# Performance work log

Hardware: AMD Instinct MI355X
Metric: run time of the kernel (lower is better)

The kernel has to match this reference:

```python
import jax, jax.numpy as jnp
import numpy as np

P = 8          # patch_size
HEADS = 4      # patch_size // 2
DIM = 256      # nf*P*P // 16
DH = DIM // HEADS


def setup_inputs() -> dict:
    key = jax.random.key(0)
    ks = jax.random.split(key, 8)
    B, N, C, H, W = 8, 1, 64, 256, 256
    Np = (H // P) * (W // P)           # 1024
    patch_dim = C * P * P              # 4096
    s = 0.02
    return {
        "x": jax.random.normal(ks[0], (B, N, C, H, W), jnp.float32),
        "W_embed": jax.random.normal(ks[1], (DIM, patch_dim), jnp.float32) * s,
        "b_embed": jnp.zeros((DIM,), jnp.float32),
        "pos": jax.random.normal(ks[2], (1, Np, DIM), jnp.float32),
        "Wq": jax.random.normal(ks[3], (DIM, DIM), jnp.float32) * s,
        "Wk": jax.random.normal(ks[4], (Np, Np), jnp.float32) * s,
        "Wv": jax.random.normal(ks[5], (DIM, DIM), jnp.float32) * s,
        "Wout": jax.random.normal(ks[6], (patch_dim, DIM), jnp.float32) * s,
        "b_out": jnp.zeros((patch_dim,), jnp.float32),
    }


def reference(x, W_embed, b_embed, pos, Wq, Wk, Wv, Wout, b_out):
    B, N, C, H, W = x.shape
    Hp, Wp = H // P, W // P
    Np = Hp * Wp
    patch_dim = C * P * P
    BN = B * N

    # unfold (non-overlapping patches), column order = (C, kh, kw)
    xb = x.reshape(BN, C, Hp, P, Wp, P)
    patches = xb.transpose(0, 2, 4, 1, 3, 5).reshape(BN, Np, patch_dim)

    # linear_embed + positional embedding
    emb = jnp.einsum('bnp,dp->bnd', patches, W_embed) + b_embed + pos  # (BN, Np, DIM)

    # q: linear, split heads, mean over head-dim (AvgPool1d(dh) on length dh)
    q = jnp.einsum('bnd,ed->bne', emb, Wq)
    q = q.reshape(BN, Np, HEADS, DH).transpose(0, 2, 1, 3)  # (BN, H, Np, DH)
    q = q.mean(axis=-1)                                      # (BN, H, Np)

    # k = sigmoid(linear_k(q)); diag_embed(k) @ v == k[..., None] * v
    k = jax.nn.sigmoid(jnp.einsum('bhn,mn->bhm', q, Wk))     # (BN, H, Np)

    v = jnp.einsum('bnd,ed->bne', emb, Wv)
    v = v.reshape(BN, Np, HEADS, DH).transpose(0, 2, 1, 3)   # (BN, H, Np, DH)

    out = k[..., None] * v                                   # (BN, H, Np, DH)
    out = out.transpose(0, 2, 1, 3).reshape(BN, Np, DIM)

    out = jnp.einsum('bnd,pd->bnp', out, Wout) + b_out       # (BN, Np, patch_dim)

    # fold back to image
    out = out.reshape(BN, Hp, Wp, C, P, P).transpose(0, 3, 1, 4, 2, 5)
    out = out.reshape(B, N, C, H, W)
    return out
```

## Files before the change

kernel.cpp:

```cpp
#include <hip/hip_runtime.h>

typedef __attribute__((ext_vector_type(8))) short short8;
typedef __attribute__((ext_vector_type(4))) float f32x4;

#define LDA 72
#define QST 264
#define KST 257

__device__ __forceinline__ unsigned short f2bf(float f) {
  unsigned int u = __builtin_bit_cast(unsigned int, f);
  u += 0x7fffu + ((u >> 16) & 1u);
  return (unsigned short)(u >> 16);
}
__device__ __forceinline__ float bf2f(unsigned short us) {
  return __builtin_bit_cast(float, (unsigned int)us << 16);
}

__global__ __launch_bounds__(256) void cvt_bf16_kernel(const float* __restrict__ src,
                                                       unsigned short* __restrict__ dst,
                                                       int n4) {
  int i = blockIdx.x * 256 + threadIdx.x;
  if (i >= n4) return;
  float4 f = ((const float4*)src)[i];
  unsigned int lo = (unsigned int)f2bf(f.x) | ((unsigned int)f2bf(f.y) << 16);
  unsigned int hi = (unsigned int)f2bf(f.z) | ((unsigned int)f2bf(f.w) << 16);
  uint2 u; u.x = lo; u.y = hi;
  ((uint2*)dst)[i] = u;
}

__global__ __launch_bounds__(256) void wqr_kernel(const float* __restrict__ Wq,
                                                  float* __restrict__ WqR) {
  int idx = blockIdx.x * 256 + threadIdx.x;
  int h = idx >> 8, e = idx & 255;
  float s = 0.f;
  for (int j = 0; j < 64; ++j) s += Wq[(size_t)(h * 64 + j) * 256 + e];
  WqR[idx] = s * (1.f / 64.f);
}

__global__ __launch_bounds__(256) void gemm1_embed(
    const float* __restrict__ x, const unsigned short* __restrict__ Wb,
    const float* __restrict__ b_embed, const float* __restrict__ pos,
    unsigned short* __restrict__ emb_bf) {
  __shared__ __align__(16) unsigned short As[64 * LDA];
  __shared__ __align__(16) unsigned short Bs[128 * LDA];
  const int nt = blockIdx.x, mt = blockIdx.y;
  const int m0 = mt * 64, n0 = nt * 128;
  const int t = threadIdx.x;
  const int wave = t >> 6, lane = t & 63;
  const int wm = wave >> 1, wn = wave & 1;
  const int lr = lane & 15, lq = lane >> 4;
  f32x4 acc[2][4];
#pragma unroll
  for (int i = 0; i < 2; i++)
#pragma unroll
    for (int j = 0; j < 4; j++) acc[i][j] = f32x4{0.f, 0.f, 0.f, 0.f};

  for (int kt = 0; kt < 64; ++kt) {
    const int k0 = kt * 64;
#pragma unroll
    for (int rr = 0; rr < 2; ++rr) {
      int r = t + rr * 256;
      int m = r >> 3, krun = r & 7;
      int gm = m0 + m;
      int bn = gm >> 10, nn = gm & 1023;
      int ph = nn >> 5, pw = nn & 31;
      int k = k0 + krun * 8;
      int c = k >> 6, kh = (k >> 3) & 7;
      const float* src = x + ((size_t)((bn << 6) + c) << 16) +
                         (size_t)((ph << 3) + kh) * 256 + (pw << 3);
      float4 f0 = *(const float4*)src;
      float4 f1 = *(const float4*)(src + 4);
      short8 v;
      v[0] = (short)f2bf(f0.x); v[1] = (short)f2bf(f0.y);
      v[2] = (short)f2bf(f0.z); v[3] = (short)f2bf(f0.w);
      v[4] = (short)f2bf(f1.x); v[5] = (short)f2bf(f1.y);
      v[6] = (short)f2bf(f1.z); v[7] = (short)f2bf(f1.w);
      *(short8*)&As[m * LDA + krun * 8] = v;
    }
#pragma unroll
    for (int rr = 0; rr < 4; ++rr) {
      int r = t + rr * 256;
      int n = r >> 3, krun = r & 7;
      *(short8*)&Bs[n * LDA + krun * 8] =
          *(const short8*)(Wb + (size_t)(n0 + n) * 4096 + k0 + krun * 8);
    }
    __syncthreads();
#pragma unroll
    for (int kc = 0; kc < 2; ++kc) {
      short8 a0 = *(const short8*)&As[(wm * 32 + lr) * LDA + kc * 32 + lq * 8];
      short8 a1 = *(const short8*)&As[(wm * 32 + 16 + lr) * LDA + kc * 32 + lq * 8];
#pragma unroll
      for (int ni = 0; ni < 4; ++ni) {
        short8 b = *(const short8*)&Bs[(wn * 64 + ni * 16 + lr) * LDA + kc * 32 + lq * 8];
        acc[0][ni] = __builtin_amdgcn_mfma_f32_16x16x32_bf16(a0, b, acc[0][ni], 0, 0, 0);
        acc[1][ni] = __builtin_amdgcn_mfma_f32_16x16x32_bf16(a1, b, acc[1][ni], 0, 0, 0);
      }
    }
    __syncthreads();
  }
#pragma unroll
  for (int mi = 0; mi < 2; ++mi)
#pragma unroll
    for (int ni = 0; ni < 4; ++ni) {
      int col = n0 + wn * 64 + ni * 16 + lr;
      float be = b_embed[col];
      int rbase = m0 + wm * 32 + mi * 16 + lq * 4;
#pragma unroll
      for (int r2 = 0; r2 < 4; ++r2) {
        int row = rbase + r2;
        int n = row & 1023;
        emb_bf[(size_t)row * 256 + col] =
            f2bf(acc[mi][ni][r2] + be + pos[(size_t)n * 256 + col]);
      }
    }
}

__global__ __launch_bounds__(256) void q_kernel(const unsigned short* __restrict__ emb_bf,
                                                const float* __restrict__ WqR,
                                                float* __restrict__ q) {
  __shared__ __align__(16) unsigned short es[64 * QST];
  __shared__ float wq[1024];
  const int t = threadIdx.x;
  for (int i = t; i < 1024; i += 256) wq[i] = WqR[i];
  const int row0 = blockIdx.x * 64;
#pragma unroll
  for (int i = 0; i < 8; ++i) {
    int r = t + i * 256;
    int rr = r >> 5, c8 = r & 31;
    *(short8*)&es[rr * QST + c8 * 8] =
        *(const short8*)(emb_bf + (size_t)(row0 + rr) * 256 + c8 * 8);
  }
  __syncthreads();
  const int row = t >> 2, h = t & 3;
  const float* w = wq + h * 256;
  float s = 0.f;
#pragma unroll 4
  for (int e8 = 0; e8 < 32; ++e8) {
    short8 v = *(const short8*)&es[row * QST + e8 * 8];
#pragma unroll
    for (int j = 0; j < 8; ++j)
      s += bf2f((unsigned short)v[j]) * w[e8 * 8 + j];
  }
  int grow = row0 + row;
  int bn = grow >> 10, n = grow & 1023;
  q[(size_t)(bn * 4 + h) * 1024 + n] = s;
}

__global__ __launch_bounds__(256) void k_kernel(const float* __restrict__ q,
                                                const float* __restrict__ Wk,
                                                float* __restrict__ kk) {
  __shared__ float wks[32 * KST];
  __shared__ float qs[32 * KST];
  const int m0 = blockIdx.x * 32;
  const int t = threadIdx.x;
  const int m = t & 31, bh4 = t >> 5;
  float acc[4] = {0.f, 0.f, 0.f, 0.f};
  for (int kt = 0; kt < 4; ++kt) {
    const int k0 = kt * 256;
#pragma unroll
    for (int i = 0; i < 32; ++i) {
      int r = t + i * 256;
      int rr = r >> 8, c = r & 255;
      wks[rr * KST + c] = Wk[(size_t)(m0 + rr) * 1024 + k0 + c];
      qs[rr * KST + c] = q[(size_t)rr * 1024 + k0 + c];
    }
    __syncthreads();
    for (int k = 0; k < 256; ++k) {
      float a = wks[m * KST + k];
      acc[0] += a * qs[(bh4 * 4 + 0) * KST + k];
      acc[1] += a * qs[(bh4 * 4 + 1) * KST + k];
      acc[2] += a * qs[(bh4 * 4 + 2) * KST + k];
      acc[3] += a * qs[(bh4 * 4 + 3) * KST + k];
    }
    __syncthreads();
  }
#pragma unroll
  for (int j = 0; j < 4; ++j)
    kk[(size_t)(bh4 * 4 + j) * 1024 + m0 + m] = 1.f / (1.f + __expf(-acc[j]));
}

__global__ __launch_bounds__(256) void vgemm_kernel(
    const unsigned short* __restrict__ Abf, const unsigned short* __restrict__ Wvb,
    const float* __restrict__ kk, unsigned short* __restrict__ ov) {
  __shared__ __align__(16) unsigned short As[64 * LDA];
  __shared__ __align__(16) unsigned short Bs[64 * LDA];
  const int nt = blockIdx.x, mt = blockIdx.y;
  const int m0 = mt * 64, n0 = nt * 64;
  const int t = threadIdx.x;
  const int wave = t >> 6, lane = t & 63;
  const int wm = wave >> 1, wn = wave & 1;
  const int lr = lane & 15, lq = lane >> 4;
  f32x4 acc[2][2];
#pragma unroll
  for (int i = 0; i < 2; i++)
#pragma unroll
    for (int j = 0; j < 2; j++) acc[i][j] = f32x4{0.f, 0.f, 0.f, 0.f};

  for (int kt = 0; kt < 4; ++kt) {
    const int k0 = kt * 64;
#pragma unroll
    for (int rr = 0; rr < 2; ++rr) {
      int r = t + rr * 256;
      int m = r >> 3, krun = r & 7;
      *(short8*)&As[m * LDA + krun * 8] =
          *(const short8*)(Abf + (size_t)(m0 + m) * 256 + k0 + krun * 8);
    }
#pragma unroll
    for (int rr = 0; rr < 2; ++rr) {
      int r = t + rr * 256;
      int n = r >> 3, krun = r & 7;
      *(short8*)&Bs[n * LDA + krun * 8] =
          *(const short8*)(Wvb + (size_t)(n0 + n) * 256 + k0 + krun * 8);
    }
    __syncthreads();
#pragma unroll
    for (int kc = 0; kc < 2; ++kc) {
      short8 a0 = *(const short8*)&As[(wm * 32 + lr) * LDA + kc * 32 + lq * 8];
      short8 a1 = *(const short8*)&As[(wm * 32 + 16 + lr) * LDA + kc * 32 + lq * 8];
      short8 b0 = *(const short8*)&Bs[(wn * 32 + lr) * LDA + kc * 32 + lq * 8];
      short8 b1 = *(const short8*)&Bs[(wn * 32 + 16 + lr) * LDA + kc * 32 + lq * 8];
      acc[0][0] = __builtin_amdgcn_mfma_f32_16x16x32_bf16(a0, b0, acc[0][0], 0, 0, 0);
      acc[0][1] = __builtin_amdgcn_mfma_f32_16x16x32_bf16(a0, b1, acc[0][1], 0, 0, 0);
      acc[1][0] = __builtin_amdgcn_mfma_f32_16x16x32_bf16(a1, b0, acc[1][0], 0, 0, 0);
      acc[1][1] = __builtin_amdgcn_mfma_f32_16x16x32_bf16(a1, b1, acc[1][1], 0, 0, 0);
    }
    __syncthreads();
  }
#pragma unroll
  for (int mi = 0; mi < 2; ++mi)
#pragma unroll
    for (int ni = 0; ni < 2; ++ni) {
      int col = n0 + wn * 32 + ni * 16 + lr;
      int h = col >> 6;
      int rbase = m0 + wm * 32 + mi * 16 + lq * 4;
#pragma unroll
      for (int r2 = 0; r2 < 4; ++r2) {
        int row = rbase + r2;
        int bn = row >> 10, n = row & 1023;
        float g = kk[(size_t)(bn * 4 + h) * 1024 + n];
        ov[(size_t)row * 256 + col] = f2bf(acc[mi][ni][r2] * g);
      }
    }
}

__global__ __launch_bounds__(256) void gemm2_out(
    const unsigned short* __restrict__ Abf, const unsigned short* __restrict__ Wob,
    const float* __restrict__ b_out, float* __restrict__ out) {
  __shared__ __align__(16) unsigned short As[64 * LDA];
  __shared__ __align__(16) unsigned short Bs[64 * LDA];
  const int nt = blockIdx.x, mt = blockIdx.y;
  const int m0 = mt * 64, n0 = nt * 64;
  const int t = threadIdx.x;
  const int wave = t >> 6, lane = t & 63;
  const int wm = wave >> 1, wn = wave & 1;
  const int lr = lane & 15, lq = lane >> 4;
  f32x4 acc[2][2];
#pragma unroll
  for (int i = 0; i < 2; i++)
#pragma unroll
    for (int j = 0; j < 2; j++) acc[i][j] = f32x4{0.f, 0.f, 0.f, 0.f};

  for (int kt = 0; kt < 4; ++kt) {
    const int k0 = kt * 64;
#pragma unroll
    for (int rr = 0; rr < 2; ++rr) {
      int r = t + rr * 256;
      int m = r >> 3, krun = r & 7;
      *(short8*)&As[m * LDA + krun * 8] =
          *(const short8*)(Abf + (size_t)(m0 + m) * 256 + k0 + krun * 8);
    }
#pragma unroll
    for (int rr = 0; rr < 2; ++rr) {
      int r = t + rr * 256;
      int n = r >> 3, krun = r & 7;
      *(short8*)&Bs[n * LDA + krun * 8] =
          *(const short8*)(Wob + (size_t)(n0 + n) * 256 + k0 + krun * 8);
    }
    __syncthreads();
#pragma unroll
    for (int kc = 0; kc < 2; ++kc) {
      short8 a0 = *(const short8*)&As[(wm * 32 + lr) * LDA + kc * 32 + lq * 8];
      short8 a1 = *(const short8*)&As[(wm * 32 + 16 + lr) * LDA + kc * 32 + lq * 8];
      short8 b0 = *(const short8*)&Bs[(wn * 32 + lr) * LDA + kc * 32 + lq * 8];
      short8 b1 = *(const short8*)&Bs[(wn * 32 + 16 + lr) * LDA + kc * 32 + lq * 8];
      acc[0][0] = __builtin_amdgcn_mfma_f32_16x16x32_bf16(a0, b0, acc[0][0], 0, 0, 0);
      acc[0][1] = __builtin_amdgcn_mfma_f32_16x16x32_bf16(a0, b1, acc[0][1], 0, 0, 0);
      acc[1][0] = __builtin_amdgcn_mfma_f32_16x16x32_bf16(a1, b0, acc[1][0], 0, 0, 0);
      acc[1][1] = __builtin_amdgcn_mfma_f32_16x16x32_bf16(a1, b1, acc[1][1], 0, 0, 0);
    }
    __syncthreads();
  }
#pragma unroll
  for (int mi = 0; mi < 2; ++mi)
#pragma unroll
    for (int ni = 0; ni < 2; ++ni) {
      int p = n0 + wn * 32 + ni * 16 + lr;
      int c = p >> 6, kh = (p >> 3) & 7, kw = p & 7;
      float bo = b_out[p];
      int rbase = m0 + wm * 32 + mi * 16 + lq * 4;
#pragma unroll
      for (int r2 = 0; r2 < 4; ++r2) {
        int row = rbase + r2;
        int bn = row >> 10, nn = row & 1023;
        int ph = nn >> 5, pw = nn & 31;
        size_t addr = ((size_t)((bn << 6) + c) << 16) +
                      (size_t)((ph << 3) + kh) * 256 + (pw << 3) + kw;
        out[addr] = acc[mi][ni][r2] + bo;
      }
    }
}

extern "C" void kernel_launch(void* const* d_in, const int* in_sizes, int n_in,
                              void* d_out, int out_size, void* d_ws, size_t ws_size,
                              hipStream_t stream) {
  const float* x       = (const float*)d_in[0];
  const float* W_embed = (const float*)d_in[1];
  const float* b_embed = (const float*)d_in[2];
  const float* pos     = (const float*)d_in[3];
  const float* Wq      = (const float*)d_in[4];
  const float* Wk      = (const float*)d_in[5];
  const float* Wv      = (const float*)d_in[6];
  const float* Wout    = (const float*)d_in[7];
  const float* b_out   = (const float*)d_in[8];
  float* out = (float*)d_out;

  char* ws = (char*)d_ws;
  const size_t MB = 1024 * 1024;
  unsigned short* emb_bf = (unsigned short*)(ws);
  unsigned short* ov     = (unsigned short*)(ws + 4 * MB);
  unsigned short* Wb     = (unsigned short*)(ws + 8 * MB);
  unsigned short* Wob    = (unsigned short*)(ws + 10 * MB);
  unsigned short* Wvb    = (unsigned short*)(ws + 12 * MB);
  float* q               = (float*)(ws + 12 * MB + 131072);
  float* kk              = (float*)(ws + 12 * MB + 262144);
  float* WqR             = (float*)(ws + 12 * MB + 393216);

  cvt_bf16_kernel<<<1024, 256, 0, stream>>>(W_embed, Wb, 262144);
  cvt_bf16_kernel<<<1024, 256, 0, stream>>>(Wout, Wob, 262144);
  cvt_bf16_kernel<<<64, 256, 0, stream>>>(Wv, Wvb, 16384);
  wqr_kernel<<<4, 256, 0, stream>>>(Wq, WqR);
  gemm1_embed<<<dim3(2, 128), 256, 0, stream>>>(x, Wb, b_embed, pos, emb_bf);
  q_kernel<<<128, 256, 0, stream>>>(emb_bf, WqR, q);
  k_kernel<<<32, 256, 0, stream>>>(q, Wk, kk);
  vgemm_kernel<<<dim3(4, 128), 256, 0, stream>>>(emb_bf, Wvb, kk, ov);
  gemm2_out<<<dim3(64, 128), 256, 0, stream>>>(ov, Wob, b_out, out);
}
```

Baseline: 389.3 us.

## Split-K embed GEMM, fuse reduction with q, retile k/v/out kernels, coalesce output stores

Merges the four weight-prep launches into a single kernel. Splits the embedding GEMM four ways along K so the grid grows from 256 to 1024 blocks, then sums the partials in a new kernel that also adds bias and pos and computes q. The k kernel gets more blocks and float4 loads, vgemm uses 32-row tiles for more blocks, and gemm2 uses 128-wide tiles that are staged through shared memory so the fold back to the image is written with coalesced float4 stores. The cost is extra global traffic for the fp32 partials, about 32MB written and read.

```diff
diff --git a/kernel.cpp b/kernel.cpp
--- a/kernel.cpp
+++ b/kernel.cpp
@@ -4,8 +4,7 @@
 typedef __attribute__((ext_vector_type(4))) float f32x4;
 
 #define LDA 72
-#define QST 264
-#define KST 257
+#define KST 260
 
 __device__ __forceinline__ unsigned short f2bf(float f) {
   unsigned int u = __builtin_bit_cast(unsigned int, f);
@@ -16,11 +15,9 @@
   return __builtin_bit_cast(float, (unsigned int)us << 16);
 }
 
-__global__ __launch_bounds__(256) void cvt_bf16_kernel(const float* __restrict__ src,
-                                                       unsigned short* __restrict__ dst,
-                                                       int n4) {
-  int i = blockIdx.x * 256 + threadIdx.x;
-  if (i >= n4) return;
+__device__ __forceinline__ void cvt_block(const float* __restrict__ src,
+                                          unsigned short* __restrict__ dst, int b) {
+  int i = b * 256 + threadIdx.x;
   float4 f = ((const float4*)src)[i];
   unsigned int lo = (unsigned int)f2bf(f.x) | ((unsigned int)f2bf(f.y) << 16);
   unsigned int hi = (unsigned int)f2bf(f.z) | ((unsigned int)f2bf(f.w) << 16);
@@ -28,9 +25,16 @@
   ((uint2*)dst)[i] = u;
 }
 
-__global__ __launch_bounds__(256) void wqr_kernel(const float* __restrict__ Wq,
-                                                  float* __restrict__ WqR) {
-  int idx = blockIdx.x * 256 + threadIdx.x;
+__global__ __launch_bounds__(256) void prep_kernel(
+    const float* __restrict__ W_embed, const float* __restrict__ Wout,
+    const float* __restrict__ Wv, const float* __restrict__ Wq,
+    unsigned short* __restrict__ Wb, unsigned short* __restrict__ Wob,
+    unsigned short* __restrict__ Wvb, float* __restrict__ WqR) {
+  int b = blockIdx.x;
+  if (b < 1024) { cvt_block(W_embed, Wb, b); return; }
+  if (b < 2048) { cvt_block(Wout, Wob, b - 1024); return; }
+  if (b < 2112) { cvt_block(Wv, Wvb, b - 2048); return; }
+  int idx = (b - 2112) * 256 + threadIdx.x;
   int h = idx >> 8, e = idx & 255;
   float s = 0.f;
   for (int j = 0; j < 64; ++j) s += Wq[(size_t)(h * 64 + j) * 256 + e];
@@ -39,11 +43,10 @@
 
 __global__ __launch_bounds__(256) void gemm1_embed(
     const float* __restrict__ x, const unsigned short* __restrict__ Wb,
-    const float* __restrict__ b_embed, const float* __restrict__ pos,
-    unsigned short* __restrict__ emb_bf) {
+    float* __restrict__ part) {
   __shared__ __align__(16) unsigned short As[64 * LDA];
   __shared__ __align__(16) unsigned short Bs[128 * LDA];
-  const int nt = blockIdx.x, mt = blockIdx.y;
+  const int nt = blockIdx.x, mt = blockIdx.y, sk = blockIdx.z;
   const int m0 = mt * 64, n0 = nt * 128;
   const int t = threadIdx.x;
   const int wave = t >> 6, lane = t & 63;
@@ -55,7 +58,7 @@
 #pragma unroll
     for (int j = 0; j < 4; j++) acc[i][j] = f32x4{0.f, 0.f, 0.f, 0.f};
 
-  for (int kt = 0; kt < 64; ++kt) {
+  for (int kt = sk * 16; kt < sk * 16 + 16; ++kt) {
     const int k0 = kt * 64;
 #pragma unroll
     for (int rr = 0; rr < 2; ++rr) {
@@ -98,103 +101,192 @@
     }
     __syncthreads();
   }
+  float* pdst = part + (size_t)sk * 2097152;
 #pragma unroll
   for (int mi = 0; mi < 2; ++mi)
 #pragma unroll
     for (int ni = 0; ni < 4; ++ni) {
       int col = n0 + wn * 64 + ni * 16 + lr;
-      float be = b_embed[col];
       int rbase = m0 + wm * 32 + mi * 16 + lq * 4;
 #pragma unroll
-      for (int r2 = 0; r2 < 4; ++r2) {
-        int row = rbase + r2;
-        int n = row & 1023;
-        emb_bf[(size_t)row * 256 + col] =
-            f2bf(acc[mi][ni][r2] + be + pos[(size_t)n * 256 + col]);
-      }
-    }
-}
-
-__global__ __launch_bounds__(256) void q_kernel(const unsigned short* __restrict__ emb_bf,
-                                                const float* __restrict__ WqR,
-                                                float* __restrict__ q) {
-  __shared__ __align__(16) unsigned short es[64 * QST];
+      for (int r2 = 0; r2 < 4; ++r2)
+        pdst[(size_t)(rbase + r2) * 256 + col] = acc[mi][ni][r2];
+    }
+}
+
+__global__ __launch_bounds__(256) void finq_kernel(
+    const float* __restrict__ part, const float* __restrict__ b_embed,
+    const float* __restrict__ pos, const float* __restrict__ WqR,
+    unsigned short* __restrict__ emb_bf, float* __restrict__ q) {
   __shared__ float wq[1024];
   const int t = threadIdx.x;
   for (int i = t; i < 1024; i += 256) wq[i] = WqR[i];
-  const int row0 = blockIdx.x * 64;
-#pragma unroll
-  for (int i = 0; i < 8; ++i) {
-    int r = t + i * 256;
-    int rr = r >> 5, c8 = r & 31;
-    *(short8*)&es[rr * QST + c8 * 8] =
-        *(const short8*)(emb_bf + (size_t)(row0 + rr) * 256 + c8 * 8);
-  }
   __syncthreads();
-  const int row = t >> 2, h = t & 3;
-  const float* w = wq + h * 256;
-  float s = 0.f;
-#pragma unroll 4
-  for (int e8 = 0; e8 < 32; ++e8) {
-    short8 v = *(const short8*)&es[row * QST + e8 * 8];
-#pragma unroll
-    for (int j = 0; j < 8; ++j)
-      s += bf2f((unsigned short)v[j]) * w[e8 * 8 + j];
-  }
-  int grow = row0 + row;
-  int bn = grow >> 10, n = grow & 1023;
-  q[(size_t)(bn * 4 + h) * 1024 + n] = s;
+  const int row_l = t >> 3, seg = t & 7;
+  const int row = blockIdx.x * 32 + row_l;
+  const int bn = row >> 10, n = row & 1023;
+  const float4* p4 = (const float4*)part;
+  const float4* b4 = (const float4*)b_embed;
+  const float4* pos4 = (const float4*)pos;
+  const float4* wq4 = (const float4*)wq;
+  const int idx0 = row * 64 + seg * 8;
+
+  float4 e[8];
+#pragma unroll
+  for (int j = 0; j < 8; ++j) {
+    float4 v = p4[idx0 + j];
+    float4 v1 = p4[524288 + idx0 + j];
+    float4 v2 = p4[1048576 + idx0 + j];
+    float4 v3 = p4[1572864 + idx0 + j];
+    float4 bb = b4[seg * 8 + j];
+    float4 pp = pos4[(size_t)n * 64 + seg * 8 + j];
+    e[j].x = v.x + v1.x + v2.x + v3.x + bb.x + pp.x;
+    e[j].y = v.y + v1.y + v2.y + v3.y + bb.y + pp.y;
+    e[j].z = v.z + v1.z + v2.z + v3.z + bb.z + pp.z;
+    e[j].w = v.w + v1.w + v2.w + v3.w + bb.w + pp.w;
+  }
+  unsigned int ub[16];
+#pragma unroll
+  for (int j = 0; j < 8; ++j) {
+    ub[2 * j]     = (unsigned int)f2bf(e[j].x) | ((unsigned int)f2bf(e[j].y) << 16);
+    ub[2 * j + 1] = (unsigned int)f2bf(e[j].z) | ((unsigned int)f2bf(e[j].w) << 16);
+  }
+  uint4* dst = (uint4*)(emb_bf + (size_t)row * 256 + seg * 32);
+#pragma unroll
+  for (int j = 0; j < 4; ++j)
+    dst[j] = make_uint4(ub[4 * j], ub[4 * j + 1], ub[4 * j + 2], ub[4 * j + 3]);
+  float s[4] = {0.f, 0.f, 0.f, 0.f};
+#pragma unroll
+  for (int h = 0; h < 4; ++h)
+#pragma unroll
+    for (int j = 0; j < 8; ++j) {
+      float4 w = wq4[h * 64 + seg * 8 + j];
+      s[h] += e[j].x * w.x + e[j].y * w.y + e[j].z * w.z + e[j].w * w.w;
+    }
+#pragma unroll
+  for (int h = 0; h < 4; ++h) {
+    s[h] += __shfl_xor(s[h], 1);
+    s[h] += __shfl_xor(s[h], 2);
+    s[h] += __shfl_xor(s[h], 4);
+  }
+  if (seg == 0) {
+#pragma unroll
+    for (int h = 0; h < 4; ++h)
+      q[(size_t)(bn * 4 + h) * 1024 + n] = s[h];
+  }
 }
 
 __global__ __launch_bounds__(256) void k_kernel(const float* __restrict__ q,
                                                 const float* __restrict__ Wk,
                                                 float* __restrict__ kk) {
-  __shared__ float wks[32 * KST];
-  __shared__ float qs[32 * KST];
-  const int m0 = blockIdx.x * 32;
-  const int t = threadIdx.x;
-  const int m = t & 31, bh4 = t >> 5;
-  float acc[4] = {0.f, 0.f, 0.f, 0.f};
+  __shared__ float wk_s[8 * KST];
+  __shared__ float q_s[32 * KST];
+  const int m0 = blockIdx.x * 8;
+  const int t = threadIdx.x;
+  const int m = t & 7, bh = t >> 3;
+  const float4* wkg = (const float4*)Wk;
+  const float4* qg = (const float4*)q;
+  float acc = 0.f;
   for (int kt = 0; kt < 4; ++kt) {
     const int k0 = kt * 256;
 #pragma unroll
-    for (int i = 0; i < 32; ++i) {
-      int r = t + i * 256;
-      int rr = r >> 8, c = r & 255;
-      wks[rr * KST + c] = Wk[(size_t)(m0 + rr) * 1024 + k0 + c];
-      qs[rr * KST + c] = q[(size_t)rr * 1024 + k0 + c];
-    }
-    __syncthreads();
-    for (int k = 0; k < 256; ++k) {
-      float a = wks[m * KST + k];
-      acc[0] += a * qs[(bh4 * 4 + 0) * KST + k];
-      acc[1] += a * qs[(bh4 * 4 + 1) * KST + k];
-      acc[2] += a * qs[(bh4 * 4 + 2) * KST + k];
-      acc[3] += a * qs[(bh4 * 4 + 3) * KST + k];
-    }
-    __syncthreads();
-  }
-#pragma unroll
-  for (int j = 0; j < 4; ++j)
-    kk[(size_t)(bh4 * 4 + j) * 1024 + m0 + m] = 1.f / (1.f + __expf(-acc[j]));
+    for (int i = 0; i < 2; ++i) {
+      int idx = t + i * 256;
+      int r = idx >> 6, c4 = idx & 63;
+      *(float4*)&wk_s[r * KST + c4 * 4] = wkg[((size_t)(m0 + r) * 1024 + k0) / 4 + c4];
+    }
+#pragma unroll
+    for (int i = 0; i < 8; ++i) {
+      int idx = t + i * 256;
+      int r = idx >> 6, c4 = idx & 63;
+      *(float4*)&q_s[r * KST + c4 * 4] = qg[((size_t)r * 1024 + k0) / 4 + c4];
+    }
+    __syncthreads();
+#pragma unroll 8
+    for (int k4 = 0; k4 < 64; ++k4) {
+      float4 a = *(const float4*)&wk_s[m * KST + k4 * 4];
+      float4 b = *(const float4*)&q_s[bh * KST + k4 * 4];
+      acc += a.x * b.x + a.y * b.y + a.z * b.z + a.w * b.w;
+    }
+    __syncthreads();
+  }
+  kk[(size_t)bh * 1024 + m0 + m] = 1.f / (1.f + __expf(-acc));
 }
 
 __global__ __launch_bounds__(256) void vgemm_kernel(
     const unsigned short* __restrict__ Abf, const unsigned short* __restrict__ Wvb,
     const float* __restrict__ kk, unsigned short* __restrict__ ov) {
-  __shared__ __align__(16) unsigned short As[64 * LDA];
+  __shared__ __align__(16) unsigned short As[32 * LDA];
   __shared__ __align__(16) unsigned short Bs[64 * LDA];
   const int nt = blockIdx.x, mt = blockIdx.y;
-  const int m0 = mt * 64, n0 = nt * 64;
+  const int m0 = mt * 32, n0 = nt * 64;
+  const int t = threadIdx.x;
+  const int wave = t >> 6, lane = t & 63;
+  const int wr = wave >> 1, wc = wave & 1;
+  const int lr = lane & 15, lq = lane >> 4;
+  f32x4 acc[2];
+  acc[0] = f32x4{0.f, 0.f, 0.f, 0.f};
+  acc[1] = f32x4{0.f, 0.f, 0.f, 0.f};
+
+  for (int kt = 0; kt < 4; ++kt) {
+    const int k0 = kt * 64;
+    {
+      int m = t >> 3, krun = t & 7;
+      *(short8*)&As[m * LDA + krun * 8] =
+          *(const short8*)(Abf + (size_t)(m0 + m) * 256 + k0 + krun * 8);
+    }
+#pragma unroll
+    for (int rr = 0; rr < 2; ++rr) {
+      int r = t + rr * 256;
+      int n = r >> 3, krun = r & 7;
+      *(short8*)&Bs[n * LDA + krun * 8] =
+          *(const short8*)(Wvb + (size_t)(n0 + n) * 256 + k0 + krun * 8);
+    }
+    __syncthreads();
+#pragma unroll
+    for (int kc = 0; kc < 2; ++kc) {
+      short8 a = *(const short8*)&As[(wr * 16 + lr) * LDA + kc * 32 + lq * 8];
+#pragma unroll
+      for (int ni = 0; ni < 2; ++ni) {
+        short8 b = *(const short8*)&Bs[(wc * 32 + ni * 16 + lr) * LDA + kc * 32 + lq * 8];
+        acc[ni] = __builtin_amdgcn_mfma_f32_16x16x32_bf16(a, b, acc[ni], 0, 0, 0);
+      }
+    }
+    __syncthreads();
+  }
+#pragma unroll
+  for (int ni = 0; ni < 2; ++ni) {
+    int col = n0 + wc * 32 + ni * 16 + lr;
+    int h = col >> 6;
+    int rbase = m0 + wr * 16 + lq * 4;
+#pragma unroll
+    for (int r2 = 0; r2 < 4; ++r2) {
+      int row = rbase + r2;
+      int bn = row >> 10, n = row & 1023;
+      float g = kk[(size_t)(bn * 4 + h) * 1024 + n];
+      ov[(size_t)row * 256 + col] = f2bf(acc[ni][r2] * g);
+    }
+  }
+}
+
+#define CST 132
+__global__ __launch_bounds__(256) void gemm2_out(
+    const unsigned short* __restrict__ Abf, const unsigned short* __restrict__ Wob,
+    const float* __restrict__ b_out, float* __restrict__ out) {
+  __shared__ __align__(16) float smem[64 * CST];
+  unsigned short* As = (unsigned short*)smem;
+  unsigned short* Bs = As + 64 * LDA;
+  const int nt = blockIdx.x, mt = blockIdx.y;
+  const int m0 = mt * 64, n0 = nt * 128;
   const int t = threadIdx.x;
   const int wave = t >> 6, lane = t & 63;
   const int wm = wave >> 1, wn = wave & 1;
   const int lr = lane & 15, lq = lane >> 4;
-  f32x4 acc[2][2];
+  f32x4 acc[2][4];
 #pragma unroll
   for (int i = 0; i < 2; i++)
 #pragma unroll
-    for (int j = 0; j < 2; j++) acc[i][j] = f32x4{0.f, 0.f, 0.f, 0.f};
+    for (int j = 0; j < 4; j++) acc[i][j] = f32x4{0.f, 0.f, 0.f, 0.f};
 
   for (int kt = 0; kt < 4; ++kt) {
     const int k0 = kt * 64;
@@ -206,108 +298,57 @@
           *(const short8*)(Abf + (size_t)(m0 + m) * 256 + k0 + krun * 8);
     }
 #pragma unroll
-    for (int rr = 0; rr < 2; ++rr) {
+    for (int rr = 0; rr < 4; ++rr) {
       int r = t + rr * 256;
       int n = r >> 3, krun = r & 7;
       *(short8*)&Bs[n * LDA + krun * 8] =
-          *(const short8*)(Wvb + (size_t)(n0 + n) * 256 + k0 + krun * 8);
+          *(const short8*)(Wob + (size_t)(n0 + n) * 256 + k0 + krun * 8);
     }
     __syncthreads();
 #pragma unroll
     for (int kc = 0; kc < 2; ++kc) {
       short8 a0 = *(const short8*)&As[(wm * 32 + lr) * LDA + kc * 32 + lq * 8];
       short8 a1 = *(const short8*)&As[(wm * 32 + 16 + lr) * LDA + kc * 32 + lq * 8];
-      short8 b0 = *(const short8*)&Bs[(wn * 32 + lr) * LDA + kc * 32 + lq * 8];
-      short8 b1 = *(const short8*)&Bs[(wn * 32 + 16 + lr) * LDA + kc * 32 + lq * 8];
-      acc[0][0] = __builtin_amdgcn_mfma_f32_16x16x32_bf16(a0, b0, acc[0][0], 0, 0, 0);
-      acc[0][1] = __builtin_amdgcn_mfma_f32_16x16x32_bf16(a0, b1, acc[0][1], 0, 0, 0);
-      acc[1][0] = __builtin_amdgcn_mfma_f32_16x16x32_bf16(a1, b0, acc[1][0], 0, 0, 0);
-      acc[1][1] = __builtin_amdgcn_mfma_f32_16x16x32_bf16(a1, b1, acc[1][1], 0, 0, 0);
+#pragma unroll
+      for (int ni = 0; ni < 4; ++ni) {
+        short8 b = *(const short8*)&Bs[(wn * 64 + ni * 16 + lr) * LDA + kc * 32 + lq * 8];
+        acc[0][ni] = __builtin_amdgcn_mfma_f32_16x16x32_bf16(a0, b, acc[0][ni], 0, 0, 0);
+        acc[1][ni] = __builtin_amdgcn_mfma_f32_16x16x32_bf16(a1, b, acc[1][ni], 0, 0, 0);
+      }
     }
     __syncthreads();
   }
 #pragma unroll
   for (int mi = 0; mi < 2; ++mi)
 #pragma unroll
-    for (int ni = 0; ni < 2; ++ni) {
-      int col = n0 + wn * 32 + ni * 16 + lr;
-      int h = col >> 6;
-      int rbase = m0 + wm * 32 + mi * 16 + lq * 4;
-#pragma unroll
-      for (int r2 = 0; r2 < 4; ++r2) {
-        int row = rbase + r2;
-        int bn = row >> 10, n = row & 1023;
-        float g = kk[(size_t)(bn * 4 + h) * 1024 + n];
-        ov[(size_t)row * 256 + col] = f2bf(acc[mi][ni][r2] * g);
-      }
-    }
-}
-
-__global__ __launch_bounds__(256) void gemm2_out(
-    const unsigned short* __restrict__ Abf, const unsigned short* __restrict__ Wob,
-    const float* __restrict__ b_out, float* __restrict__ out) {
-  __shared__ __align__(16) unsigned short As[64 * LDA];
-  __shared__ __align__(16) unsigned short Bs[64 * LDA];
-  const int nt = blockIdx.x, mt = blockIdx.y;
-  const int m0 = mt * 64, n0 = nt * 64;
-  const int t = threadIdx.x;
-  const int wave = t >> 6, lane = t & 63;
-  const int wm = wave >> 1, wn = wave & 1;
-  const int lr = lane & 15, lq = lane >> 4;
-  f32x4 acc[2][2];
-#pragma unroll
-  for (int i = 0; i < 2; i++)
-#pragma unroll
-    for (int j = 0; j < 2; j++) acc[i][j] = f32x4{0.f, 0.f, 0.f, 0.f};
-
-  for (int kt = 0; kt < 4; ++kt) {
-    const int k0 = kt * 64;
-#pragma unroll
-    for (int rr = 0; rr < 2; ++rr) {
-      int r = t + rr * 256;
-      int m = r >> 3, krun = r & 7;
-      *(short8*)&As[m * LDA + krun * 8] =
-          *(const short8*)(Abf + (size_t)(m0 + m) * 256 + k0 + krun * 8);
-    }
-#pragma unroll
-    for (int rr = 0; rr < 2; ++rr) {
-      int r = t + rr * 256;
-      int n = r >> 3, krun = r & 7;
-      *(short8*)&Bs[n * LDA + krun * 8] =
-          *(const short8*)(Wob + (size_t)(n0 + n) * 256 + k0 + krun * 8);
-    }
-    __syncthreads();
-#pragma unroll
-    for (int kc = 0; kc < 2; ++kc) {
-      short8 a0 = *(const short8*)&As[(wm * 32 + lr) * LDA + kc * 32 + lq * 8];
-      short8 a1 = *(const short8*)&As[(wm * 32 + 16 + lr) * LDA + kc * 32 + lq * 8];
-      short8 b0 = *(const short8*)&Bs[(wn * 32 + lr) * LDA + kc * 32 + lq * 8];
-      short8 b1 = *(const short8*)&Bs[(wn * 32 + 16 + lr) * LDA + kc * 32 + lq * 8];
-      acc[0][0] = __builtin_amdgcn_mfma_f32_16x16x32_bf16(a0, b0, acc[0][0], 0, 0, 0);
-      acc[0][1] = __builtin_amdgcn_mfma_f32_16x16x32_bf16(a0, b1, acc[0][1], 0, 0, 0);
-      acc[1][0] = __builtin_amdgcn_mfma_f32_16x16x32_bf16(a1, b0, acc[1][0], 0, 0, 0);
-      acc[1][1] = __builtin_amdgcn_mfma_f32_16x16x32_bf16(a1, b1, acc[1][1], 0, 0, 0);
-    }
-    __syncthreads();
-  }
-#pragma unroll
-  for (int mi = 0; mi < 2; ++mi)
-#pragma unroll
-    for (int ni = 0; ni < 2; ++ni) {
-      int p = n0 + wn * 32 + ni * 16 + lr;
-      int c = p >> 6, kh = (p >> 3) & 7, kw = p & 7;
-      float bo = b_out[p];
-      int rbase = m0 + wm * 32 + mi * 16 + lq * 4;
-#pragma unroll
-      for (int r2 = 0; r2 < 4; ++r2) {
-        int row = rbase + r2;
-        int bn = row >> 10, nn = row & 1023;
-        int ph = nn >> 5, pw = nn & 31;
-        size_t addr = ((size_t)((bn << 6) + c) << 16) +
-                      (size_t)((ph << 3) + kh) * 256 + (pw << 3) + kw;
-        out[addr] = acc[mi][ni][r2] + bo;
-      }
-    }
+    for (int ni = 0; ni < 4; ++ni) {
+      int pl = wn * 64 + ni * 16 + lr;
+      int mb = wm * 32 + mi * 16 + lq * 4;
+#pragma unroll
+      for (int r2 = 0; r2 < 4; ++r2)
+        smem[(mb + r2) * CST + pl] = acc[mi][ni][r2];
+    }
+  __syncthreads();
+  const int bn = m0 >> 10;
+  const int ph0 = (m0 & 1023) >> 5;
+  const int c0 = n0 >> 6;
+#pragma unroll
+  for (int i = 0; i < 8; ++i) {
+    int idx4 = t + i * 256;
+    int kw4 = idx4 & 1;
+    int pw = (idx4 >> 1) & 31;
+    int kh = (idx4 >> 6) & 7;
+    int c2 = (idx4 >> 9) & 1;
+    int ph = (idx4 >> 10) & 1;
+    int m_local = ph * 32 + pw;
+    int p_local = c2 * 64 + kh * 8 + kw4 * 4;
+    float4 v = *(const float4*)&smem[m_local * CST + p_local];
+    float4 bo = *(const float4*)(b_out + n0 + p_local);
+    v.x += bo.x; v.y += bo.y; v.z += bo.z; v.w += bo.w;
+    size_t addr = ((size_t)((bn << 6) + c0 + c2) << 16) +
+                  (size_t)(((ph0 + ph) << 3) + kh) * 256 + (pw << 3) + kw4 * 4;
+    *(float4*)(out + addr) = v;
+  }
 }
 
 extern "C" void kernel_launch(void* const* d_in, const int* in_sizes, int n_in,
@@ -326,22 +367,20 @@
 
   char* ws = (char*)d_ws;
   const size_t MB = 1024 * 1024;
-  unsigned short* emb_bf = (unsigned short*)(ws);
-  unsigned short* ov     = (unsigned short*)(ws + 4 * MB);
-  unsigned short* Wb     = (unsigned short*)(ws + 8 * MB);
-  unsigned short* Wob    = (unsigned short*)(ws + 10 * MB);
-  unsigned short* Wvb    = (unsigned short*)(ws + 12 * MB);
-  float* q               = (float*)(ws + 12 * MB + 131072);
-  float* kk              = (float*)(ws + 12 * MB + 262144);
-  float* WqR             = (float*)(ws + 12 * MB + 393216);
-
-  cvt_bf16_kernel<<<1024, 256, 0, stream>>>(W_embed, Wb, 262144);
-  cvt_bf16_kernel<<<1024, 256, 0, stream>>>(Wout, Wob, 262144);
-  cvt_bf16_kernel<<<64, 256, 0, stream>>>(Wv, Wvb, 16384);
-  wqr_kernel<<<4, 256, 0, stream>>>(Wq, WqR);
-  gemm1_embed<<<dim3(2, 128), 256, 0, stream>>>(x, Wb, b_embed, pos, emb_bf);
-  q_kernel<<<128, 256, 0, stream>>>(emb_bf, WqR, q);
-  k_kernel<<<32, 256, 0, stream>>>(q, Wk, kk);
-  vgemm_kernel<<<dim3(4, 128), 256, 0, stream>>>(emb_bf, Wvb, kk, ov);
-  gemm2_out<<<dim3(64, 128), 256, 0, stream>>>(ov, Wob, b_out, out);
-}
+  float* part            = (float*)(ws);
+  unsigned short* ov     = (unsigned short*)(ws);
+  unsigned short* emb_bf = (unsigned short*)(ws + 32 * MB);
+  unsigned short* Wb     = (unsigned short*)(ws + 36 * MB);
+  unsigned short* Wob    = (unsigned short*)(ws + 38 * MB);
+  unsigned short* Wvb    = (unsigned short*)(ws + 40 * MB);
+  float* q               = (float*)(ws + 40 * MB + 131072);
+  float* kk              = (float*)(ws + 40 * MB + 262144);
+  float* WqR             = (float*)(ws + 40 * MB + 393216);
+
+  prep_kernel<<<2116, 256, 0, stream>>>(W_embed, Wout, Wv, Wq, Wb, Wob, Wvb, WqR);
+  gemm1_embed<<<dim3(2, 128, 4), 256, 0, stream>>>(x, Wb, part);
+  finq_kernel<<<256, 256, 0, stream>>>(part, b_embed, pos, WqR, emb_bf, q);
+  k_kernel<<<128, 256, 0, stream>>>(q, Wk, kk);
+  vgemm_kernel<<<dim3(4, 256), 256, 0, stream>>>(emb_bf, Wvb, kk, ov);
+  gemm2_out<<<dim3(32, 128), 256, 0, stream>>>(ov, Wob, b_out, out);
+}
```

Measured after the change: 357.4 us. 8.2% less time.
